# Optimization experiments

Hardware: AMD Instinct MI355X
Metric: run time of the kernel (lower is better)

## Reference

```python
import jax, jax.numpy as jnp
import numpy as np

B, S, H, HEADS, STEP = 128, 256, 128, 8, 1


def setup_inputs() -> dict:
    key = jax.random.key(0)
    ks = jax.random.split(key, 20)
    rn = lambda k, shape: jax.random.normal(k, shape, dtype=jnp.float32) * 0.1
    return {
        "A": jax.random.uniform(ks[0], (B, S, 2 * S), dtype=jnp.float32),
        "hidden": jax.random.normal(ks[1], (B, S, H), dtype=jnp.float32),
        "mask": jnp.ones((B, S), dtype=jnp.int32),
        "w_ih": rn(ks[2], (3 * H, 2 * H)),
        "w_hh": rn(ks[3], (3 * H, H)),
        "b_ih": rn(ks[4], (3 * H,)),
        "b_hh": rn(ks[5], (3 * H,)),
        "b_iah": rn(ks[6], (H,)),
        "b_oah": rn(ks[7], (H,)),
        "W_ein": rn(ks[8], (H, H)), "b_ein": rn(ks[9], (H,)),
        "W_eout": rn(ks[10], (H, H)), "b_eout": rn(ks[11], (H,)),
        "W_q0": rn(ks[12], (H, H)), "b_q0": rn(ks[13], (H,)),
        "W_q1": rn(ks[14], (H, H)), "b_q1": rn(ks[15], (H,)),
        "W_q2": rn(ks[16], (H, H)), "b_q2": rn(ks[17], (H,)),
    }


def _forward(A, hidden, mask, w_ih, w_hh, b_ih, b_hh, b_iah, b_oah,
             W_ein, b_ein, W_eout, b_eout, W_q0, b_q0, W_q1, b_q1, W_q2, b_q2):
    b, s, h = hidden.shape
    dk = h // HEADS
    # ---- GNN: gated graph propagation (GRU cell over adjacency messages) ----
    for _ in range(STEP):
        msg_in = A[:, :, :s] @ (hidden @ W_ein.T + b_ein) + b_iah    # [B,S,H]
        msg_out = A[:, :, s:] @ (hidden @ W_eout.T + b_eout) + b_oah  # [B,S,H]
        inputs = jnp.concatenate([msg_in, msg_out], axis=2)           # [B,S,2H]
        gi = inputs @ w_ih.T + b_ih                                   # [B,S,3H]
        gh = hidden @ w_hh.T + b_hh                                   # [B,S,3H]
        i_r, i_i, i_n = jnp.split(gi, 3, axis=2)
        h_r, h_i, h_n = jnp.split(gh, 3, axis=2)
        resetgate = jax.nn.sigmoid(i_r + h_r)
        inputgate = jax.nn.sigmoid(i_i + h_i)
        newgate = jnp.tanh(i_n + resetgate * h_n)
        hidden = hidden - inputgate * (hidden - newgate)
    # ---- query: hidden state of the last valid item in each session ----
    last_idx = jnp.sum(mask, axis=1) - 1
    ht1 = hidden[jnp.arange(b), last_idx]                             # [B,H]
    # ---- LastAttenion: sigmoid score + double softmax readout ----
    q0 = (ht1 @ W_q0.T + b_q0).reshape(b, HEADS, dk)                  # [B,h,dk]
    q1 = (hidden @ W_q1.T + b_q1).reshape(b, s, HEADS, dk).transpose(0, 2, 1, 3)
    q2 = (hidden @ W_q2.T + b_q2).reshape(b, s, HEADS, dk).transpose(0, 2, 1, 3)
    # q0 is expanded over the query axis, so every score row is identical
    alpha = jax.nn.sigmoid(jnp.einsum('bhd,bhjd->bhj', q0, q1))        # [B,h,S]
    alpha = jnp.broadcast_to(alpha[:, :, None, :], (b, HEADS, s, s))   # [B,h,S,S]
    alpha = jax.nn.softmax(alpha, axis=-1)
    row_keep = (mask > 0)[:, None, :, None]                            # [B,1,S,1]
    alpha = jnp.where(row_keep, alpha, -jnp.inf)
    alpha = jax.nn.softmax(2.0 * alpha, axis=1)                        # over heads
    alpha = jnp.where(row_keep, alpha, 0.0)  # guard fully-masked rows (torch would NaN)
    x = jnp.einsum('bhij,bhjd->bhid', alpha, q2)                       # [B,h,S,dk]
    x = x.transpose(0, 2, 1, 3).reshape(b, s, h)                       # [B,S,H]
    a = jnp.sum(x * mask[:, :, None].astype(x.dtype), axis=1)          # [B,H]
    return a


def reference(A, hidden, mask, w_ih, w_hh, b_ih, b_hh, b_iah, b_oah,
              W_ein, b_ein, W_eout, b_eout, W_q0, b_q0, W_q1, b_q1, W_q2, b_q2):
    return _forward(A, hidden, mask, w_ih, w_hh, b_ih, b_hh, b_iah, b_oah,
                    W_ein, b_ein, W_eout, b_eout, W_q0, b_q0, W_q1, b_q1, W_q2, b_q2)
```

## Files before the change

kernel.cpp:

```cpp
#include <hip/hip_runtime.h>
#include <cstdint>
#include <cstddef>

#define BB   128
#define SS   256
#define HH   128
#define NH   8
#define DKK  16

typedef unsigned short u16;
typedef __attribute__((ext_vector_type(8))) short   sh8;
typedef __attribute__((ext_vector_type(4))) float   f32x4;

__device__ __forceinline__ float sigmoidf_(float x) { return 1.f / (1.f + expf(-x)); }

__device__ __forceinline__ u16 f2bf(float x) {
    union { float f; unsigned int u; } v; v.f = x;
    unsigned int r = (v.u + 0x7fffu + ((v.u >> 16) & 1u)) >> 16;
    return (u16)r;
}
__device__ __forceinline__ float bf2f(u16 u) {
    union { unsigned int u; float f; } v; v.u = ((unsigned int)u) << 16;
    return v.f;
}
__device__ __forceinline__ float bflo(unsigned u) {
    union { unsigned u; float f; } v; v.u = u << 16; return v.f;
}
__device__ __forceinline__ float bfhi(unsigned u) {
    union { unsigned u; float f; } v; v.u = u & 0xffff0000u; return v.f;
}

#define BKk 32
#define PK  40
#define LP  136

template<int XMODE, int OMODE>
__global__ __launch_bounds__(256) void gemm_mfma(
    const void* __restrict__ Xa, const void* __restrict__ Xc, int ldx, int ldx1, int ksplit,
    long long sXb, long long sXh,
    const u16* __restrict__ Bw, int ldb, long long sBb, long long sBh,
    const float* __restrict__ bias,
    void* __restrict__ Out, long long ldo, long long sOb, long long sOh,
    int K, const u16* __restrict__ hid)
{
    __shared__ __align__(16) char smem[2 * 128 * PK * 2];
    u16* As = (u16*)smem;
    u16* Bs = (u16*)(smem + 128 * PK * 2);

    const int t  = threadIdx.x;
    const int bm = blockIdx.x * 128;
    const int bn = blockIdx.y * 128;
    const long long zb = blockIdx.z >> 1, zh = blockIdx.z & 1;

    const u16* Bp = Bw + zb * sBb + zh * sBh;

    const int wave = t >> 6, lane = t & 63;
    const int wr = (wave >> 1) * 64, wc = (wave & 1) * 64;
    const int fm = lane & 15, fq = lane >> 4;

    f32x4 acc[4][4] = {};

    const int r0  = t >> 2, kk0 = (t & 3) * 8;
    const int r1  = t >> 3, kk1 = (t & 7) * 4;

    uint4  px0, px1, pb0, pb1;
    float4 pf0, pf1, pf2, pf3;

#define LOADX(K0)                                                                    \
    if (XMODE == 1) {                                                                \
        const float* Xf_ = (const float*)Xa + zb * sXb + zh * sXh;                   \
        const float* xp_ = Xf_ + (long long)(bm + r1) * ldx + (K0) + kk1;            \
        pf0 = *(const float4*)(xp_);                                                 \
        pf1 = *(const float4*)(xp_ + 32LL * ldx);                                    \
        pf2 = *(const float4*)(xp_ + 64LL * ldx);                                    \
        pf3 = *(const float4*)(xp_ + 96LL * ldx);                                    \
    } else if (XMODE == 2 && (K0) >= ksplit) {                                       \
        const u16* xp_ = (const u16*)Xc + (long long)(bm + r0) * ldx1                \
                         + ((K0) - ksplit) + kk0;                                    \
        px0 = *(const uint4*)(xp_);                                                  \
        px1 = *(const uint4*)(xp_ + 64LL * ldx1);                                    \
    } else {                                                                         \
        const u16* xp_ = (const u16*)Xa + (long long)(bm + r0) * ldx + (K0) + kk0;   \
        px0 = *(const uint4*)(xp_);                                                  \
        px1 = *(const uint4*)(xp_ + 64LL * ldx);                                     \
    }

#define LOADB(K0)                                                                    \
    {                                                                                \
        const u16* bp_ = Bp + (long long)(bn + r0) * ldb + (K0) + kk0;               \
        pb0 = *(const uint4*)(bp_);                                                  \
        pb1 = *(const uint4*)(bp_ + 64LL * ldb);                                     \
    }

    LOADX(0)
    LOADB(0)

    for (int k0 = 0; k0 < K; k0 += BKk) {
        if (XMODE == 1) {
            ushort4 w0 = { f2bf(pf0.x), f2bf(pf0.y), f2bf(pf0.z), f2bf(pf0.w) };
            ushort4 w1 = { f2bf(pf1.x), f2bf(pf1.y), f2bf(pf1.z), f2bf(pf1.w) };
            ushort4 w2 = { f2bf(pf2.x), f2bf(pf2.y), f2bf(pf2.z), f2bf(pf2.w) };
            ushort4 w3 = { f2bf(pf3.x), f2bf(pf3.y), f2bf(pf3.z), f2bf(pf3.w) };
            *(ushort4*)&As[(r1     ) * PK + kk1] = w0;
            *(ushort4*)&As[(r1 + 32) * PK + kk1] = w1;
            *(ushort4*)&As[(r1 + 64) * PK + kk1] = w2;
            *(ushort4*)&As[(r1 + 96) * PK + kk1] = w3;
        } else {
            *(uint4*)&As[(r0     ) * PK + kk0] = px0;
            *(uint4*)&As[(r0 + 64) * PK + kk0] = px1;
        }
        *(uint4*)&Bs[(r0     ) * PK + kk0] = pb0;
        *(uint4*)&Bs[(r0 + 64) * PK + kk0] = pb1;
        __syncthreads();

        if (k0 + BKk < K) {
            LOADX(k0 + BKk)
            LOADB(k0 + BKk)
        }

        sh8 af[4], bfr[4];
        #pragma unroll
        for (int i = 0; i < 4; i++) af[i]  = *(const sh8*)&As[(wr + i * 16 + fm) * PK + fq * 8];
        #pragma unroll
        for (int j = 0; j < 4; j++) bfr[j] = *(const sh8*)&Bs[(wc + j * 16 + fm) * PK + fq * 8];
        #pragma unroll
        for (int i = 0; i < 4; i++)
            #pragma unroll
            for (int j = 0; j < 4; j++)
                acc[i][j] = __builtin_amdgcn_mfma_f32_16x16x32_bf16(af[i], bfr[j], acc[i][j], 0, 0, 0);
        __syncthreads();
    }
#undef LOADX
#undef LOADB

    if (OMODE != 3) {
        u16* O  = (u16*)Out + zb * sOb + zh * sOh;
        u16* Ls = (u16*)smem;
        #pragma unroll
        for (int hf = 0; hf < 2; hf++) {
            if (hf) __syncthreads();
            if (OMODE == 1) {
                if (wr == hf * 64) {
                    #pragma unroll
                    for (int i = 0; i < 4; i++)
                        #pragma unroll
                        for (int j = 0; j < 4; j++) {
                            const int cl = wc + j * 16 + fm;
                            const float bj = bias ? bias[bn + cl] : 0.f;
                            #pragma unroll
                            for (int r = 0; r < 4; r++)
                                Ls[(i * 16 + fq * 4 + r) * LP + cl] = f2bf(acc[i][j][r] + bj);
                        }
                }
            } else {
                if (wc == hf * 64) {
                    #pragma unroll
                    for (int i = 0; i < 4; i++)
                        #pragma unroll
                        for (int j = 0; j < 4; j++) {
                            const int cl = j * 16 + fm;
                            const float bj = bias ? bias[bn + hf * 64 + cl] : 0.f;
                            ushort4 w = { f2bf(acc[i][j][0] + bj), f2bf(acc[i][j][1] + bj),
                                          f2bf(acc[i][j][2] + bj), f2bf(acc[i][j][3] + bj) };
                            *(ushort4*)&Ls[cl * LP + wr + i * 16 + fq * 4] = w;
                        }
                }
            }
            __syncthreads();
            const int ro = t >> 2;
            #pragma unroll
            for (int rr = 0; rr < 4; rr++) {
                const int c0 = ((t & 3) + rr * 4) * 8;
                uint4 w = *(const uint4*)&Ls[ro * LP + c0];
                if (OMODE == 1)
                    *(uint4*)&O[(long long)(bm + hf * 64 + ro) * ldo + bn + c0] = w;
                else
                    *(uint4*)&O[(long long)(bn + hf * 64 + ro) * ldo + bm + c0] = w;
            }
        }
    } else {
        float* g4s = (float*)smem;
        const int chbase = bn >> 2;
        const int s_t = t >> 3;
        const int cq  = t & 7;
        u16* O = (u16*)Out;
        const int sbase = (wr ? 16 : 0) + fq * 4;
        #pragma unroll
        for (int i = 0; i < 4; i++) {
            #pragma unroll
            for (int j = 0; j < 4; j++) {
                const int q = wc + j * 16 + fm;
                const float bj = bias[bn + q];
                #pragma unroll
                for (int r = 0; r < 4; r++)
                    g4s[(sbase + r) * 132 + q] = acc[i][j][r] + bj;
            }
            __syncthreads();
            {
                const int grow = bm + i * 16 + (s_t < 16 ? s_t : s_t + 48);
                const ushort4 hv = *(const ushort4*)&hid[(long long)grow * HH + chbase + 4 * cq];
                const float hvv[4] = { bf2f(hv.x), bf2f(hv.y), bf2f(hv.z), bf2f(hv.w) };
                ushort4 w;
                u16* wp = (u16*)&w;
                #pragma unroll
                for (int m = 0; m < 4; m++) {
                    f32x4 gv = *(const f32x4*)&g4s[s_t * 132 + 16 * cq + 4 * m];
                    float rg = sigmoidf_(gv[0]);
                    float ig = sigmoidf_(gv[1]);
                    float ng = tanhf(gv[2] + rg * gv[3]);
                    wp[m] = f2bf(hvv[m] - ig * (hvv[m] - ng));
                }
                *(ushort4*)&O[(long long)grow * ldo + chbase + 4 * cq] = w;
            }
            __syncthreads();
        }
    }
}

__global__ __launch_bounds__(256) void k_prepw(
    const float* __restrict__ hidden, u16* __restrict__ h_bf,
    const float* __restrict__ w_ih, const float* __restrict__ w_hh,
    const float* __restrict__ b_ih, const float* __restrict__ b_hh,
    const float* __restrict__ b_iah, const float* __restrict__ b_oah,
    const float* __restrict__ W_ein, const float* __restrict__ b_ein,
    const float* __restrict__ W_eout, const float* __restrict__ b_eout,
    const float* __restrict__ W_q1, const float* __restrict__ b_q1,
    const float* __restrict__ W_q2, const float* __restrict__ b_q2,
    u16* __restrict__ W2bf, float* __restrict__ bias2,
    u16* __restrict__ Wcat, float* __restrict__ biascat,
    u16* __restrict__ Wq12, float* __restrict__ biasq12)
{
    int idx = blockIdx.x * 256 + threadIdx.x;
    {
        float4 v = ((const float4*)hidden)[idx];
        ushort4 w = { f2bf(v.x), f2bf(v.y), f2bf(v.z), f2bf(v.w) };
        ((ushort4*)h_bf)[idx] = w;
    }
    if (idx < 512 * 384) {
        int np = idx / 384, kk = idx % 384;
        int c = np >> 2, g = np & 3;
        float v;
        if (g < 2)       v = (kk < 256) ? w_ih[(g * 128 + c) * 256 + kk]
                                        : w_hh[(g * 128 + c) * 128 + kk - 256];
        else if (g == 2) v = (kk < 256) ? w_ih[(256 + c) * 256 + kk] : 0.f;
        else             v = (kk < 256) ? 0.f : w_hh[(256 + c) * 128 + kk - 256];
        W2bf[idx] = f2bf(v);
    }
    if (idx < 256 * 128) {
        int n = idx >> 7, k = idx & 127;
        Wcat[idx] = f2bf(n < 128 ? W_ein[n * 128 + k] : W_eout[(n - 128) * 128 + k]);
        Wq12[idx] = f2bf(n < 128 ? W_q1[n * 128 + k]  : W_q2[(n - 128) * 128 + k]);
    }
    if (idx < 512) {
        int np = idx, c = np >> 2, g = np & 3;
        float s;
        if (g < 2)       s = b_ih[g * 128 + c] + b_hh[g * 128 + c];
        else if (g == 2) s = b_ih[256 + c];
        else             s = b_hh[256 + c];
        if (g < 3) {
            int n = (g < 2) ? g * 128 + c : 256 + c;
            for (int k = 0; k < 128; k++)
                s += w_ih[n * 256 + k] * b_iah[k] + w_ih[n * 256 + 128 + k] * b_oah[k];
        }
        bias2[np] = s;
    }
    if (idx < 256) {
        biascat[idx] = idx < 128 ? b_ein[idx] : b_eout[idx - 128];
        biasq12[idx] = idx < 128 ? b_q1[idx]  : b_q2[idx - 128];
    }
}

__global__ __launch_bounds__(1024) void k_tail(
    const u16* __restrict__ hnew_bf, const int* __restrict__ mask,
    const u16* __restrict__ q12, const float* __restrict__ Wq0,
    const float* __restrict__ bq0, float* __restrict__ out)
{
    const int b = blockIdx.x, chb = blockIdx.y, t = threadIdx.x;
    __shared__ float red[1024];
    __shared__ float red2[1024][2];
    __shared__ float hs[HH];
    __shared__ float q0s[HH];
    __shared__ float p_s[NH][SS];
    __shared__ float w_s[NH][SS];
    __shared__ int s_nv;

    if (t < 256) {
        int v = mask[b * SS + t];
        #pragma unroll
        for (int m = 1; m < 64; m <<= 1) v += __shfl_xor(v, m, 64);
        if ((t & 63) == 0) red[t >> 6] = (float)v;
    }
    __syncthreads();
    if (t == 0) s_nv = (int)(red[0] + red[1] + red[2] + red[3]);
    __syncthreads();
    const int nv = s_nv;
    const int last = (nv - 1) & (SS - 1);

    if (t < HH) hs[t] = bf2f(hnew_bf[((size_t)b * SS + last) * HH + t]);
    __syncthreads();

    {
        const int n = t & 127, kh = t >> 7;
        const float* w = Wq0 + (size_t)n * HH + kh * 16;
        const float* h = hs + kh * 16;
        float s = 0.f;
        #pragma unroll
        for (int k = 0; k < 16; k++) s += h[k] * w[k];
        red[t] = s;
    }
    __syncthreads();
    if (t < HH) {
        float s = bq0[t];
        #pragma unroll
        for (int kh = 0; kh < 8; kh++) s += red[kh * 128 + t];
        q0s[t] = s;
    }
    __syncthreads();

    {
        const int j = t >> 2, q = t & 3;
        const u16* q1r = q12 + ((size_t)b * SS + j) * 256 + q * 32;
        uint4 va = *(const uint4*)(q1r);
        uint4 vb = *(const uint4*)(q1r + 8);
        uint4 vc = *(const uint4*)(q1r + 16);
        uint4 vd = *(const uint4*)(q1r + 24);
        const float* qa = q0s + q * 32;
        float s0 = qa[0]  * bflo(va.x) + qa[1]  * bfhi(va.x)
                 + qa[2]  * bflo(va.y) + qa[3]  * bfhi(va.y)
                 + qa[4]  * bflo(va.z) + qa[5]  * bfhi(va.z)
                 + qa[6]  * bflo(va.w) + qa[7]  * bfhi(va.w)
                 + qa[8]  * bflo(vb.x) + qa[9]  * bfhi(vb.x)
                 + qa[10] * bflo(vb.y) + qa[11] * bfhi(vb.y)
                 + qa[12] * bflo(vb.z) + qa[13] * bfhi(vb.z)
                 + qa[14] * bflo(vb.w) + qa[15] * bfhi(vb.w);
        float s1 = qa[16] * bflo(vc.x) + qa[17] * bfhi(vc.x)
                 + qa[18] * bflo(vc.y) + qa[19] * bfhi(vc.y)
                 + qa[20] * bflo(vc.z) + qa[21] * bfhi(vc.z)
                 + qa[22] * bflo(vc.w) + qa[23] * bfhi(vc.w)
                 + qa[24] * bflo(vd.x) + qa[25] * bfhi(vd.x)
                 + qa[26] * bflo(vd.y) + qa[27] * bfhi(vd.y)
                 + qa[28] * bflo(vd.z) + qa[29] * bfhi(vd.z)
                 + qa[30] * bflo(vd.w) + qa[31] * bfhi(vd.w);
        p_s[2 * q][j]     = sigmoidf_(s0);
        p_s[2 * q + 1][j] = sigmoidf_(s1);
    }
    __syncthreads();

    if (t < 256) {
        const int h = t >> 5, l = t & 31;
        float v[8], m = -1e30f;
        #pragma unroll
        for (int u = 0; u < 8; u++) { v[u] = p_s[h][l * 8 + u]; m = fmaxf(m, v[u]); }
        #pragma unroll
        for (int msk = 1; msk < 32; msk <<= 1) m = fmaxf(m, __shfl_xor(m, msk, 32));
        float sum = 0.f;
        #pragma unroll
        for (int u = 0; u < 8; u++) { v[u] = expf(v[u] - m); sum += v[u]; }
        #pragma unroll
        for (int msk = 1; msk < 32; msk <<= 1) sum += __shfl_xor(sum, msk, 32);
        const float inv = 1.f / sum;
        #pragma unroll
        for (int u = 0; u < 8; u++) p_s[h][l * 8 + u] = v[u] * inv;
    }
    __syncthreads();

    if (t < 256) {
        float e[NH], den = 0.f;
        #pragma unroll
        for (int h = 0; h < NH; h++) { e[h] = expf(2.f * p_s[h][t]); den += e[h]; }
        const float inv = 1.f / den;
        #pragma unroll
        for (int h = 0; h < NH; h++) w_s[h][t] = e[h] * inv;
    }
    __syncthreads();

    {
        const int cp = t & 31, jq = t >> 5;
        const int col = chb * 64 + cp * 2;
        const int h0 = col >> 4;
        const u16* q2b = q12 + (size_t)b * SS * 256 + 128 + col;
        float a0 = 0.f, a1 = 0.f;
        #pragma unroll
        for (int u = 0; u < 8; u++) {
            const int j = jq * 8 + u;
            const unsigned v = *(const unsigned*)&q2b[(size_t)j * 256];
            const float w = w_s[h0][j];
            a0 += w * bflo(v);
            a1 += w * bfhi(v);
        }
        red2[t][0] = a0;
        red2[t][1] = a1;
    }
    __syncthreads();
    if (t < 64) {
        const int cp2 = t >> 1, par = t & 1;
        float s = 0.f;
        #pragma unroll
        for (int q = 0; q < 32; q++) s += red2[q * 32 + cp2][par];
        out[(size_t)b * HH + chb * 64 + cp2 * 2 + par] = s * (float)nv;
    }
}

extern "C" void kernel_launch(void* const* d_in, const int* in_sizes, int n_in,
                              void* d_out, int out_size, void* d_ws, size_t ws_size,
                              hipStream_t stream)
{
    const float* A      = (const float*)d_in[0];
    const float* hidden = (const float*)d_in[1];
    const int*   mask   = (const int*)d_in[2];
    const float* w_ih   = (const float*)d_in[3];
    const float* w_hh   = (const float*)d_in[4];
    const float* b_ih   = (const float*)d_in[5];
    const float* b_hh   = (const float*)d_in[6];
    const float* b_iah  = (const float*)d_in[7];
    const float* b_oah  = (const float*)d_in[8];
    const float* W_ein  = (const float*)d_in[9];
    const float* b_ein  = (const float*)d_in[10];
    const float* W_eout = (const float*)d_in[11];
    const float* b_eout = (const float*)d_in[12];
    const float* W_q0   = (const float*)d_in[13];
    const float* b_q0   = (const float*)d_in[14];
    const float* W_q1   = (const float*)d_in[15];
    const float* b_q1   = (const float*)d_in[16];
    const float* W_q2   = (const float*)d_in[17];
    const float* b_q2   = (const float*)d_in[18];
    float* out = (float*)d_out;
    char* ws = (char*)d_ws;

    u16*   Et      = (u16*)(ws + 0);
    u16*   Mbuf    = (u16*)(ws + 16777216);
    u16*   q12bf   = (u16*)(ws + 0);
    u16*   hnew_bf = (u16*)(ws + 33554432);
    u16*   h_bf    = (u16*)(ws + 41943040);
    u16*   W2bf    = (u16*)(ws + 50331648);
    u16*   Wcat    = (u16*)(ws + 50724864);
    u16*   Wq12    = (u16*)(ws + 50790400);
    float* bias2   = (float*)(ws + 50855936);
    float* biascat = (float*)(ws + 50857984);
    float* biasq12 = (float*)(ws + 50859008);

    k_prepw<<<4096, 256, 0, stream>>>(hidden, h_bf,
                                      w_ih, w_hh, b_ih, b_hh, b_iah, b_oah,
                                      W_ein, b_ein, W_eout, b_eout,
                                      W_q1, b_q1, W_q2, b_q2,
                                      W2bf, bias2, Wcat, biascat, Wq12, biasq12);

    gemm_mfma<0, 2><<<dim3(256, 2, 1), 256, 0, stream>>>(
        h_bf, nullptr, HH, 0, 0, 0, 0,
        Wcat, HH, 0, 0, biascat,
        Et, 32768, 0, 0, HH, nullptr);

    gemm_mfma<1, 1><<<dim3(2, 1, 256), 256, 0, stream>>>(
        A, nullptr, 512, 0, 0, 131072LL, 256LL,
        Et, 32768, 256LL, 128LL * 32768LL, nullptr,
        Mbuf, 256, 65536LL, 128LL, SS, nullptr);

    gemm_mfma<2, 3><<<dim3(256, 4, 1), 256, 0, stream>>>(
        Mbuf, h_bf, 256, HH, 256, 0, 0,
        W2bf, 384, 0, 0, bias2,
        hnew_bf, HH, 0, 0, 384, h_bf);

    gemm_mfma<0, 1><<<dim3(256, 2, 1), 256, 0, stream>>>(
        hnew_bf, nullptr, HH, 0, 0, 0, 0,
        Wq12, HH, 0, 0, biasq12,
        q12bf, 256, 0, 0, HH, nullptr);

    k_tail<<<dim3(BB, 2), 1024, 0, stream>>>(hnew_bf, mask, q12bf, W_q0, b_q0, out);
}
```

Measured before the change: 221.5 us.

## Double-buffer LDS tiles and widen GEMM K-tile to 64

Doubles the K step of the MFMA GEMM main loop from 32 to 64 and keeps two LDS buffers. The next tile is committed into the idle buffer after the MFMAs, which removes one of the two barriers per iteration and halves the iteration count. The cost is much more LDS per block (about 72 KB versus 20 KB) and more registers for prefetch, which may lower occupancy. It also assumes K is a multiple of 64 and that ksplit is aligned to 64.

```diff
diff --git a/kernel.cpp b/kernel.cpp
--- a/kernel.cpp
+++ b/kernel.cpp
@@ -30,9 +30,11 @@
     union { unsigned u; float f; } v; v.u = u & 0xffff0000u; return v.f;
 }
 
-#define BKk 32
-#define PK  40
-#define LP  136
+#define BKk  64
+#define PKB  72
+#define ABUF (128 * PKB)
+#define BUFH (2 * ABUF)
+#define LP   136
 
 template<int XMODE, int OMODE>
 __global__ __launch_bounds__(256) void gemm_mfma(
@@ -43,9 +45,8 @@
     void* __restrict__ Out, long long ldo, long long sOb, long long sOh,
     int K, const u16* __restrict__ hid)
 {
-    __shared__ __align__(16) char smem[2 * 128 * PK * 2];
-    u16* As = (u16*)smem;
-    u16* Bs = (u16*)(smem + 128 * PK * 2);
+    __shared__ __align__(16) char smem[2 * BUFH * 2];
+    u16* base = (u16*)smem;
 
     const int t  = threadIdx.x;
     const int bm = blockIdx.x * 128;
@@ -60,78 +61,124 @@
 
     f32x4 acc[4][4] = {};
 
-    const int r0  = t >> 2, kk0 = (t & 3) * 8;
-    const int r1  = t >> 3, kk1 = (t & 7) * 4;
-
-    uint4  px0, px1, pb0, pb1;
-    float4 pf0, pf1, pf2, pf3;
+    const int rs = t >> 3, kcs = (t & 7) * 8;
+    const int rf = t >> 4, cf  = (t & 15) * 4;
+
+    uint4  px0, px1, px2, px3, pb0, pb1, pb2, pb3;
+    float4 pf0, pf1, pf2, pf3, pf4, pf5, pf6, pf7;
 
 #define LOADX(K0)                                                                    \
     if (XMODE == 1) {                                                                \
         const float* Xf_ = (const float*)Xa + zb * sXb + zh * sXh;                   \
-        const float* xp_ = Xf_ + (long long)(bm + r1) * ldx + (K0) + kk1;            \
+        const float* xp_ = Xf_ + (long long)(bm + rf) * ldx + (K0) + cf;             \
         pf0 = *(const float4*)(xp_);                                                 \
-        pf1 = *(const float4*)(xp_ + 32LL * ldx);                                    \
-        pf2 = *(const float4*)(xp_ + 64LL * ldx);                                    \
-        pf3 = *(const float4*)(xp_ + 96LL * ldx);                                    \
+        pf1 = *(const float4*)(xp_ +  16LL * ldx);                                   \
+        pf2 = *(const float4*)(xp_ +  32LL * ldx);                                   \
+        pf3 = *(const float4*)(xp_ +  48LL * ldx);                                   \
+        pf4 = *(const float4*)(xp_ +  64LL * ldx);                                   \
+        pf5 = *(const float4*)(xp_ +  80LL * ldx);                                   \
+        pf6 = *(const float4*)(xp_ +  96LL * ldx);                                   \
+        pf7 = *(const float4*)(xp_ + 112LL * ldx);                                   \
     } else if (XMODE == 2 && (K0) >= ksplit) {                                       \
-        const u16* xp_ = (const u16*)Xc + (long long)(bm + r0) * ldx1                \
-                         + ((K0) - ksplit) + kk0;                                    \
+        const u16* xp_ = (const u16*)Xc + (long long)(bm + rs) * ldx1               \
+                         + ((K0) - ksplit) + kcs;                                    \
         px0 = *(const uint4*)(xp_);                                                  \
-        px1 = *(const uint4*)(xp_ + 64LL * ldx1);                                    \
+        px1 = *(const uint4*)(xp_ + 32LL * ldx1);                                    \
+        px2 = *(const uint4*)(xp_ + 64LL * ldx1);                                    \
+        px3 = *(const uint4*)(xp_ + 96LL * ldx1);                                    \
     } else {                                                                         \
-        const u16* xp_ = (const u16*)Xa + (long long)(bm + r0) * ldx + (K0) + kk0;   \
+        const u16* xp_ = (const u16*)Xa + (long long)(bm + rs) * ldx + (K0) + kcs;   \
         px0 = *(const uint4*)(xp_);                                                  \
-        px1 = *(const uint4*)(xp_ + 64LL * ldx);                                     \
+        px1 = *(const uint4*)(xp_ + 32LL * ldx);                                     \
+        px2 = *(const uint4*)(xp_ + 64LL * ldx);                                     \
+        px3 = *(const uint4*)(xp_ + 96LL * ldx);                                     \
     }
 
 #define LOADB(K0)                                                                    \
     {                                                                                \
-        const u16* bp_ = Bp + (long long)(bn + r0) * ldb + (K0) + kk0;               \
+        const u16* bp_ = Bp + (long long)(bn + rs) * ldb + (K0) + kcs;               \
         pb0 = *(const uint4*)(bp_);                                                  \
-        pb1 = *(const uint4*)(bp_ + 64LL * ldb);                                     \
-    }
+        pb1 = *(const uint4*)(bp_ + 32LL * ldb);                                     \
+        pb2 = *(const uint4*)(bp_ + 64LL * ldb);                                     \
+        pb3 = *(const uint4*)(bp_ + 96LL * ldb);                                     \
+    }
+
+#define COMMIT(Ad, Bd)                                                               \
+    if (XMODE == 1) {                                                                \
+        ushort4 w0 = { f2bf(pf0.x), f2bf(pf0.y), f2bf(pf0.z), f2bf(pf0.w) };         \
+        ushort4 w1 = { f2bf(pf1.x), f2bf(pf1.y), f2bf(pf1.z), f2bf(pf1.w) };         \
+        ushort4 w2 = { f2bf(pf2.x), f2bf(pf2.y), f2bf(pf2.z), f2bf(pf2.w) };         \
+        ushort4 w3 = { f2bf(pf3.x), f2bf(pf3.y), f2bf(pf3.z), f2bf(pf3.w) };         \
+        ushort4 w4 = { f2bf(pf4.x), f2bf(pf4.y), f2bf(pf4.z), f2bf(pf4.w) };         \
+        ushort4 w5 = { f2bf(pf5.x), f2bf(pf5.y), f2bf(pf5.z), f2bf(pf5.w) };         \
+        ushort4 w6 = { f2bf(pf6.x), f2bf(pf6.y), f2bf(pf6.z), f2bf(pf6.w) };         \
+        ushort4 w7 = { f2bf(pf7.x), f2bf(pf7.y), f2bf(pf7.z), f2bf(pf7.w) };         \
+        *(ushort4*)&(Ad)[(rf      ) * PKB + cf] = w0;                                \
+        *(ushort4*)&(Ad)[(rf +  16) * PKB + cf] = w1;                                \
+        *(ushort4*)&(Ad)[(rf +  32) * PKB + cf] = w2;                                \
+        *(ushort4*)&(Ad)[(rf +  48) * PKB + cf] = w3;                                \
+        *(ushort4*)&(Ad)[(rf +  64) * PKB + cf] = w4;                                \
+        *(ushort4*)&(Ad)[(rf +  80) * PKB + cf] = w5;                                \
+        *(ushort4*)&(Ad)[(rf +  96) * PKB + cf] = w6;                                \
+        *(ushort4*)&(Ad)[(rf + 112) * PKB + cf] = w7;                                \
+    } else {                                                                         \
+        *(uint4*)&(Ad)[(rs     ) * PKB + kcs] = px0;                                 \
+        *(uint4*)&(Ad)[(rs + 32) * PKB + kcs] = px1;                                 \
+        *(uint4*)&(Ad)[(rs + 64) * PKB + kcs] = px2;                                 \
+        *(uint4*)&(Ad)[(rs + 96) * PKB + kcs] = px3;                                 \
+    }                                                                                \
+    *(uint4*)&(Bd)[(rs     ) * PKB + kcs] = pb0;                                     \
+    *(uint4*)&(Bd)[(rs + 32) * PKB + kcs] = pb1;                                     \
+    *(uint4*)&(Bd)[(rs + 64) * PKB + kcs] = pb2;                                     \
+    *(uint4*)&(Bd)[(rs + 96) * PKB + kcs] = pb3;
+
+    const int nt = K / BKk;
+    int cur = 0;
 
     LOADX(0)
     LOADB(0)
-
-    for (int k0 = 0; k0 < K; k0 += BKk) {
-        if (XMODE == 1) {
-            ushort4 w0 = { f2bf(pf0.x), f2bf(pf0.y), f2bf(pf0.z), f2bf(pf0.w) };
-            ushort4 w1 = { f2bf(pf1.x), f2bf(pf1.y), f2bf(pf1.z), f2bf(pf1.w) };
-            ushort4 w2 = { f2bf(pf2.x), f2bf(pf2.y), f2bf(pf2.z), f2bf(pf2.w) };
-            ushort4 w3 = { f2bf(pf3.x), f2bf(pf3.y), f2bf(pf3.z), f2bf(pf3.w) };
-            *(ushort4*)&As[(r1     ) * PK + kk1] = w0;
-            *(ushort4*)&As[(r1 + 32) * PK + kk1] = w1;
-            *(ushort4*)&As[(r1 + 64) * PK + kk1] = w2;
-            *(ushort4*)&As[(r1 + 96) * PK + kk1] = w3;
-        } else {
-            *(uint4*)&As[(r0     ) * PK + kk0] = px0;
-            *(uint4*)&As[(r0 + 64) * PK + kk0] = px1;
-        }
-        *(uint4*)&Bs[(r0     ) * PK + kk0] = pb0;
-        *(uint4*)&Bs[(r0 + 64) * PK + kk0] = pb1;
-        __syncthreads();
-
-        if (k0 + BKk < K) {
-            LOADX(k0 + BKk)
-            LOADB(k0 + BKk)
-        }
-
-        sh8 af[4], bfr[4];
-        #pragma unroll
-        for (int i = 0; i < 4; i++) af[i]  = *(const sh8*)&As[(wr + i * 16 + fm) * PK + fq * 8];
-        #pragma unroll
-        for (int j = 0; j < 4; j++) bfr[j] = *(const sh8*)&Bs[(wc + j * 16 + fm) * PK + fq * 8];
-        #pragma unroll
-        for (int i = 0; i < 4; i++)
+    {
+        u16* Ad = base;
+        u16* Bd = base + ABUF;
+        COMMIT(Ad, Bd)
+    }
+    __syncthreads();
+
+    for (int tt = 0; tt < nt; ++tt) {
+        if (tt + 1 < nt) {
+            LOADX((tt + 1) * BKk)
+            LOADB((tt + 1) * BKk)
+        }
+
+        const u16* Ac = base + cur * BUFH;
+        const u16* Bc = Ac + ABUF;
+        #pragma unroll
+        for (int ks = 0; ks < 2; ks++) {
+            sh8 af[4], bfr[4];
+            #pragma unroll
+            for (int i = 0; i < 4; i++)
+                af[i]  = *(const sh8*)&Ac[(wr + i * 16 + fm) * PKB + ks * 32 + fq * 8];
             #pragma unroll
             for (int j = 0; j < 4; j++)
-                acc[i][j] = __builtin_amdgcn_mfma_f32_16x16x32_bf16(af[i], bfr[j], acc[i][j], 0, 0, 0);
+                bfr[j] = *(const sh8*)&Bc[(wc + j * 16 + fm) * PKB + ks * 32 + fq * 8];
+            #pragma unroll
+            for (int i = 0; i < 4; i++)
+                #pragma unroll
+                for (int j = 0; j < 4; j++)
+                    acc[i][j] = __builtin_amdgcn_mfma_f32_16x16x32_bf16(af[i], bfr[j], acc[i][j], 0, 0, 0);
+        }
+
+        if (tt + 1 < nt) {
+            u16* Ad = base + (cur ^ 1) * BUFH;
+            u16* Bd = Ad + ABUF;
+            COMMIT(Ad, Bd)
+        }
         __syncthreads();
+        cur ^= 1;
     }
 #undef LOADX
 #undef LOADB
+#undef COMMIT
 
     if (OMODE != 3) {
         u16* O  = (u16*)Out + zb * sOb + zh * sOh;
```

After: 218.9 us. About the same (-1.1%).

## Double-buffer the GRU gate GEMM with BK=64 and drop LDS-staged epilogue

Applied to the files above, without the earlier changes.

Adds a new gemm_dbuf kernel for the fused gate GEMM (OMODE 3). It uses two shared-memory buffers with a K tile of 64, so each step needs one barrier instead of two and the next tile's global loads overlap the current MFMAs. The generic gemm_mfma epilogue for OMODE 1/2 now writes bf16 results straight from registers to global memory instead of staging them through LDS. That removes the barriers but gives less coalesced, scattered 2-byte stores. The larger LDS footprint may reduce occupancy.

```diff
diff --git a/kernel.cpp b/kernel.cpp
--- a/kernel.cpp
+++ b/kernel.cpp
@@ -32,7 +32,6 @@
 
 #define BKk 32
 #define PK  40
-#define LP  136
 
 template<int XMODE, int OMODE>
 __global__ __launch_bounds__(256) void gemm_mfma(
@@ -66,7 +65,7 @@
     uint4  px0, px1, pb0, pb1;
     float4 pf0, pf1, pf2, pf3;
 
-#define LOADX(K0)                                                                    \
+#define LOADX32(K0)                                                                  \
     if (XMODE == 1) {                                                                \
         const float* Xf_ = (const float*)Xa + zb * sXb + zh * sXh;                   \
         const float* xp_ = Xf_ + (long long)(bm + r1) * ldx + (K0) + kk1;            \
@@ -85,15 +84,15 @@
         px1 = *(const uint4*)(xp_ + 64LL * ldx);                                     \
     }
 
-#define LOADB(K0)                                                                    \
+#define LOADB32(K0)                                                                  \
     {                                                                                \
         const u16* bp_ = Bp + (long long)(bn + r0) * ldb + (K0) + kk0;               \
         pb0 = *(const uint4*)(bp_);                                                  \
         pb1 = *(const uint4*)(bp_ + 64LL * ldb);                                     \
     }
 
-    LOADX(0)
-    LOADB(0)
+    LOADX32(0)
+    LOADB32(0)
 
     for (int k0 = 0; k0 < K; k0 += BKk) {
         if (XMODE == 1) {
@@ -114,8 +113,8 @@
         __syncthreads();
 
         if (k0 + BKk < K) {
-            LOADX(k0 + BKk)
-            LOADB(k0 + BKk)
+            LOADX32(k0 + BKk)
+            LOADB32(k0 + BKk)
         }
 
         sh8 af[4], bfr[4];
@@ -130,55 +129,149 @@
                 acc[i][j] = __builtin_amdgcn_mfma_f32_16x16x32_bf16(af[i], bfr[j], acc[i][j], 0, 0, 0);
         __syncthreads();
     }
-#undef LOADX
-#undef LOADB
-
-    if (OMODE != 3) {
-        u16* O  = (u16*)Out + zb * sOb + zh * sOh;
-        u16* Ls = (u16*)smem;
-        #pragma unroll
-        for (int hf = 0; hf < 2; hf++) {
-            if (hf) __syncthreads();
+#undef LOADX32
+#undef LOADB32
+
+    #pragma unroll
+    for (int j = 0; j < 4; j++) {
+        const int col = bn + wc + j * 16 + fm;
+        const float bj = bias ? bias[col] : 0.f;
+        #pragma unroll
+        for (int i = 0; i < 4; i++) {
+            const int row0 = bm + wr + i * 16 + fq * 4;
             if (OMODE == 1) {
-                if (wr == hf * 64) {
-                    #pragma unroll
-                    for (int i = 0; i < 4; i++)
-                        #pragma unroll
-                        for (int j = 0; j < 4; j++) {
-                            const int cl = wc + j * 16 + fm;
-                            const float bj = bias ? bias[bn + cl] : 0.f;
-                            #pragma unroll
-                            for (int r = 0; r < 4; r++)
-                                Ls[(i * 16 + fq * 4 + r) * LP + cl] = f2bf(acc[i][j][r] + bj);
-                        }
-                }
+                u16* O = (u16*)Out + zb * sOb + zh * sOh;
+                #pragma unroll
+                for (int r = 0; r < 4; r++)
+                    O[(long long)(row0 + r) * ldo + col] = f2bf(acc[i][j][r] + bj);
             } else {
-                if (wc == hf * 64) {
-                    #pragma unroll
-                    for (int i = 0; i < 4; i++)
-                        #pragma unroll
-                        for (int j = 0; j < 4; j++) {
-                            const int cl = j * 16 + fm;
-                            const float bj = bias ? bias[bn + hf * 64 + cl] : 0.f;
-                            ushort4 w = { f2bf(acc[i][j][0] + bj), f2bf(acc[i][j][1] + bj),
-                                          f2bf(acc[i][j][2] + bj), f2bf(acc[i][j][3] + bj) };
-                            *(ushort4*)&Ls[cl * LP + wr + i * 16 + fq * 4] = w;
-                        }
-                }
+                u16* O = (u16*)Out + zb * sOb + zh * sOh;
+                ushort4 w = { f2bf(acc[i][j][0] + bj), f2bf(acc[i][j][1] + bj),
+                              f2bf(acc[i][j][2] + bj), f2bf(acc[i][j][3] + bj) };
+                *(ushort4*)&O[(long long)col * ldo + row0] = w;
             }
-            __syncthreads();
-            const int ro = t >> 2;
+        }
+    }
+}
+
+#define BKD  64
+#define PKB  72
+#define ABUF (128 * PKB)
+#define BUFH (2 * ABUF)
+
+template<int XMODE, int OMODE>
+__global__ __launch_bounds__(256) void gemm_dbuf(
+    const void* __restrict__ Xa, const void* __restrict__ Xc, int ldx, int ldx1, int ksplit,
+    long long sXb, long long sXh,
+    const u16* __restrict__ Bw, int ldb, long long sBb, long long sBh,
+    const float* __restrict__ bias,
+    void* __restrict__ Out, long long ldo, long long sOb, long long sOh,
+    int K, const u16* __restrict__ hid)
+{
+    __shared__ __align__(16) char smem[2 * BUFH * 2];
+    u16* base = (u16*)smem;
+
+    const int t  = threadIdx.x;
+    const int bm = blockIdx.x * 128;
+    const int bn = blockIdx.y * 128;
+    const long long zb = blockIdx.z >> 1, zh = blockIdx.z & 1;
+
+    const u16* Bp = Bw + zb * sBb + zh * sBh;
+
+    const int wave = t >> 6, lane = t & 63;
+    const int wr = (wave >> 1) * 64, wc = (wave & 1) * 64;
+    const int fm = lane & 15, fq = lane >> 4;
+
+    f32x4 acc[4][4] = {};
+
+    const int rs = t >> 3, kcs = (t & 7) * 8;
+
+    uint4  px0, px1, px2, px3, pb0, pb1, pb2, pb3;
+
+#define LOADX64(K0)                                                                  \
+    if (XMODE == 2 && (K0) >= ksplit) {                                              \
+        const u16* xp_ = (const u16*)Xc + (long long)(bm + rs) * ldx1               \
+                         + ((K0) - ksplit) + kcs;                                    \
+        px0 = *(const uint4*)(xp_);                                                  \
+        px1 = *(const uint4*)(xp_ + 32LL * ldx1);                                    \
+        px2 = *(const uint4*)(xp_ + 64LL * ldx1);                                    \
+        px3 = *(const uint4*)(xp_ + 96LL * ldx1);                                    \
+    } else {                                                                         \
+        const u16* xp_ = (const u16*)Xa + (long long)(bm + rs) * ldx + (K0) + kcs;   \
+        px0 = *(const uint4*)(xp_);                                                  \
+        px1 = *(const uint4*)(xp_ + 32LL * ldx);                                     \
+        px2 = *(const uint4*)(xp_ + 64LL * ldx);                                     \
+        px3 = *(const uint4*)(xp_ + 96LL * ldx);                                     \
+    }
+
+#define LOADB64(K0)                                                                  \
+    {                                                                                \
+        const u16* bp_ = Bp + (long long)(bn + rs) * ldb + (K0) + kcs;               \
+        pb0 = *(const uint4*)(bp_);                                                  \
+        pb1 = *(const uint4*)(bp_ + 32LL * ldb);                                     \
+        pb2 = *(const uint4*)(bp_ + 64LL * ldb);                                     \
+        pb3 = *(const uint4*)(bp_ + 96LL * ldb);                                     \
+    }
+
+#define COMMIT64(Ad, Bd)                                                             \
+    *(uint4*)&(Ad)[(rs     ) * PKB + kcs] = px0;                                     \
+    *(uint4*)&(Ad)[(rs + 32) * PKB + kcs] = px1;                                     \
+    *(uint4*)&(Ad)[(rs + 64) * PKB + kcs] = px2;                                     \
+    *(uint4*)&(Ad)[(rs + 96) * PKB + kcs] = px3;                                     \
+    *(uint4*)&(Bd)[(rs     ) * PKB + kcs] = pb0;                                     \
+    *(uint4*)&(Bd)[(rs + 32) * PKB + kcs] = pb1;                                     \
+    *(uint4*)&(Bd)[(rs + 64) * PKB + kcs] = pb2;                                     \
+    *(uint4*)&(Bd)[(rs + 96) * PKB + kcs] = pb3;
+
+    const int nt = K / BKD;
+    int cur = 0;
+
+    LOADX64(0)
+    LOADB64(0)
+    {
+        u16* Ad = base;
+        u16* Bd = base + ABUF;
+        COMMIT64(Ad, Bd)
+    }
+    __syncthreads();
+
+    for (int tt = 0; tt < nt; ++tt) {
+        if (tt + 1 < nt) {
+            LOADX64((tt + 1) * BKD)
+            LOADB64((tt + 1) * BKD)
+        }
+
+        const u16* Ac = base + cur * BUFH;
+        const u16* Bc = Ac + ABUF;
+        #pragma unroll
+        for (int ks = 0; ks < 2; ks++) {
+            sh8 af[4], bfr[4];
             #pragma unroll
-            for (int rr = 0; rr < 4; rr++) {
-                const int c0 = ((t & 3) + rr * 4) * 8;
-                uint4 w = *(const uint4*)&Ls[ro * LP + c0];
-                if (OMODE == 1)
-                    *(uint4*)&O[(long long)(bm + hf * 64 + ro) * ldo + bn + c0] = w;
-                else
-                    *(uint4*)&O[(long long)(bn + hf * 64 + ro) * ldo + bm + c0] = w;
-            }
-        }
-    } else {
+            for (int i = 0; i < 4; i++)
+                af[i]  = *(const sh8*)&Ac[(wr + i * 16 + fm) * PKB + ks * 32 + fq * 8];
+            #pragma unroll
+            for (int j = 0; j < 4; j++)
+                bfr[j] = *(const sh8*)&Bc[(wc + j * 16 + fm) * PKB + ks * 32 + fq * 8];
+            #pragma unroll
+            for (int i = 0; i < 4; i++)
+                #pragma unroll
+                for (int j = 0; j < 4; j++)
+                    acc[i][j] = __builtin_amdgcn_mfma_f32_16x16x32_bf16(af[i], bfr[j], acc[i][j], 0, 0, 0);
+        }
+
+        if (tt + 1 < nt) {
+            u16* Ad = base + (cur ^ 1) * BUFH;
+            u16* Bd = Ad + ABUF;
+            COMMIT64(Ad, Bd)
+        }
+        __syncthreads();
+        cur ^= 1;
+    }
+#undef LOADX64
+#undef LOADB64
+#undef COMMIT64
+
+    {
         float* g4s = (float*)smem;
         const int chbase = bn >> 2;
         const int s_t = t >> 3;
@@ -455,7 +548,7 @@
         Et, 32768, 256LL, 128LL * 32768LL, nullptr,
         Mbuf, 256, 65536LL, 128LL, SS, nullptr);
 
-    gemm_mfma<2, 3><<<dim3(256, 4, 1), 256, 0, stream>>>(
+    gemm_dbuf<2, 3><<<dim3(256, 4, 1), 256, 0, stream>>>(
         Mbuf, h_bf, 256, HH, 256, 0, 0,
         W2bf, 384, 0, 0, bias2,
         hnew_bf, HH, 0, 0, 384, h_bf);
```

Result: faster. 215.3 us (-2.8%).

## Fuse adjacency message GEMM with GRU gate GEMM into one kernel

Applied to the files above, without the earlier changes.

Replaces the separate A@E message GEMM and the gate GEMM with a single kernel that keeps each 64-row message tile in LDS and immediately multiplies it by the GRU weights, applying the gate nonlinearity in the epilogue. This removes the Mbuf round trip through global memory and one launch. The generic GEMM epilogue also drops its LDS-staged coalesced store in favour of direct per-element global stores. In exchange the fused kernel uses about 80KB of LDS per block, which limits occupancy, and the direct stores are less coalesced.

```diff
diff --git a/kernel.cpp b/kernel.cpp
--- a/kernel.cpp
+++ b/kernel.cpp
@@ -32,7 +32,6 @@
 
 #define BKk 32
 #define PK  40
-#define LP  136
 
 template<int XMODE, int OMODE>
 __global__ __launch_bounds__(256) void gemm_mfma(
@@ -66,7 +65,7 @@
     uint4  px0, px1, pb0, pb1;
     float4 pf0, pf1, pf2, pf3;
 
-#define LOADX(K0)                                                                    \
+#define LOADX32(K0)                                                                  \
     if (XMODE == 1) {                                                                \
         const float* Xf_ = (const float*)Xa + zb * sXb + zh * sXh;                   \
         const float* xp_ = Xf_ + (long long)(bm + r1) * ldx + (K0) + kk1;            \
@@ -85,15 +84,15 @@
         px1 = *(const uint4*)(xp_ + 64LL * ldx);                                     \
     }
 
-#define LOADB(K0)                                                                    \
+#define LOADB32(K0)                                                                  \
     {                                                                                \
         const u16* bp_ = Bp + (long long)(bn + r0) * ldb + (K0) + kk0;               \
         pb0 = *(const uint4*)(bp_);                                                  \
         pb1 = *(const uint4*)(bp_ + 64LL * ldb);                                     \
     }
 
-    LOADX(0)
-    LOADB(0)
+    LOADX32(0)
+    LOADB32(0)
 
     for (int k0 = 0; k0 < K; k0 += BKk) {
         if (XMODE == 1) {
@@ -114,8 +113,8 @@
         __syncthreads();
 
         if (k0 + BKk < K) {
-            LOADX(k0 + BKk)
-            LOADB(k0 + BKk)
+            LOADX32(k0 + BKk)
+            LOADB32(k0 + BKk)
         }
 
         sh8 af[4], bfr[4];
@@ -130,91 +129,228 @@
                 acc[i][j] = __builtin_amdgcn_mfma_f32_16x16x32_bf16(af[i], bfr[j], acc[i][j], 0, 0, 0);
         __syncthreads();
     }
-#undef LOADX
-#undef LOADB
-
-    if (OMODE != 3) {
-        u16* O  = (u16*)Out + zb * sOb + zh * sOh;
-        u16* Ls = (u16*)smem;
-        #pragma unroll
-        for (int hf = 0; hf < 2; hf++) {
-            if (hf) __syncthreads();
+#undef LOADX32
+#undef LOADB32
+
+    #pragma unroll
+    for (int j = 0; j < 4; j++) {
+        const int col = bn + wc + j * 16 + fm;
+        const float bj = bias ? bias[col] : 0.f;
+        #pragma unroll
+        for (int i = 0; i < 4; i++) {
+            const int row0 = bm + wr + i * 16 + fq * 4;
             if (OMODE == 1) {
-                if (wr == hf * 64) {
-                    #pragma unroll
-                    for (int i = 0; i < 4; i++)
-                        #pragma unroll
-                        for (int j = 0; j < 4; j++) {
-                            const int cl = wc + j * 16 + fm;
-                            const float bj = bias ? bias[bn + cl] : 0.f;
-                            #pragma unroll
-                            for (int r = 0; r < 4; r++)
-                                Ls[(i * 16 + fq * 4 + r) * LP + cl] = f2bf(acc[i][j][r] + bj);
-                        }
-                }
-            } else {
-                if (wc == hf * 64) {
-                    #pragma unroll
-                    for (int i = 0; i < 4; i++)
-                        #pragma unroll
-                        for (int j = 0; j < 4; j++) {
-                            const int cl = j * 16 + fm;
-                            const float bj = bias ? bias[bn + hf * 64 + cl] : 0.f;
-                            ushort4 w = { f2bf(acc[i][j][0] + bj), f2bf(acc[i][j][1] + bj),
-                                          f2bf(acc[i][j][2] + bj), f2bf(acc[i][j][3] + bj) };
-                            *(ushort4*)&Ls[cl * LP + wr + i * 16 + fq * 4] = w;
-                        }
-                }
-            }
-            __syncthreads();
-            const int ro = t >> 2;
-            #pragma unroll
-            for (int rr = 0; rr < 4; rr++) {
-                const int c0 = ((t & 3) + rr * 4) * 8;
-                uint4 w = *(const uint4*)&Ls[ro * LP + c0];
-                if (OMODE == 1)
-                    *(uint4*)&O[(long long)(bm + hf * 64 + ro) * ldo + bn + c0] = w;
-                else
-                    *(uint4*)&O[(long long)(bn + hf * 64 + ro) * ldo + bm + c0] = w;
-            }
-        }
-    } else {
-        float* g4s = (float*)smem;
-        const int chbase = bn >> 2;
-        const int s_t = t >> 3;
-        const int cq  = t & 7;
-        u16* O = (u16*)Out;
-        const int sbase = (wr ? 16 : 0) + fq * 4;
-        #pragma unroll
-        for (int i = 0; i < 4; i++) {
-            #pragma unroll
-            for (int j = 0; j < 4; j++) {
-                const int q = wc + j * 16 + fm;
-                const float bj = bias[bn + q];
+                u16* O = (u16*)Out + zb * sOb + zh * sOh;
                 #pragma unroll
                 for (int r = 0; r < 4; r++)
-                    g4s[(sbase + r) * 132 + q] = acc[i][j][r] + bj;
+                    O[(long long)(row0 + r) * ldo + col] = f2bf(acc[i][j][r] + bj);
+            } else {
+                u16* O = (u16*)Out + zb * sOb + zh * sOh;
+                ushort4 w = { f2bf(acc[i][j][0] + bj), f2bf(acc[i][j][1] + bj),
+                              f2bf(acc[i][j][2] + bj), f2bf(acc[i][j][3] + bj) };
+                *(ushort4*)&O[(long long)col * ldo + row0] = w;
+            }
+        }
+    }
+}
+
+#define MGP 392
+#define SGP 40
+
+__global__ __launch_bounds__(256) void k_msg_gates(
+    const float* __restrict__ A,
+    const u16*   __restrict__ Et,
+    const u16*   __restrict__ h_bf,
+    const u16*   __restrict__ W2bf,
+    const float* __restrict__ bias2,
+    u16*         __restrict__ hnew)
+{
+    __shared__ __align__(16) char smem[80896];
+    u16*   Mloc = (u16*)smem;
+    u16*   As   = (u16*)(smem + 50176);
+    u16*   Bs   = (u16*)(smem + 60416);
+    u16*   Ws   = (u16*)(smem + 50176);
+    float* Gs   = (float*)(smem + 50176);
+
+    const int t  = threadIdx.x;
+    const int r0 = blockIdx.x * 64;
+    const int b  = blockIdx.x >> 2;
+
+    const int wave = t >> 6, lane = t & 63;
+    const int fm = lane & 15, fq = lane >> 4;
+    const int zh = wave >> 1;
+    const int wn = wave * 64;
+
+    const f32x4 fz = { 0.f, 0.f, 0.f, 0.f };
+    f32x4 acc[4][4];
+
+    {
+        const int hrow = t >> 2, cb = (t & 3) * 32;
+        const u16* hp = h_bf + (long long)(r0 + hrow) * HH + cb;
+        uint4 h0 = *(const uint4*)(hp);
+        uint4 h1 = *(const uint4*)(hp + 8);
+        uint4 h2 = *(const uint4*)(hp + 16);
+        uint4 h3 = *(const uint4*)(hp + 24);
+        *(uint4*)&Mloc[hrow * MGP + 256 + cb     ] = h0;
+        *(uint4*)&Mloc[hrow * MGP + 256 + cb + 8 ] = h1;
+        *(uint4*)&Mloc[hrow * MGP + 256 + cb + 16] = h2;
+        *(uint4*)&Mloc[hrow * MGP + 256 + cb + 24] = h3;
+    }
+
+    const int arow = t >> 1, acol = (t & 1) * 16;
+    const int arl  = arow & 63, ah = arow >> 6;
+
+    float4 qa0, qa1, qa2, qa3;
+    uint4  qe0, qe1, qe2, qe3;
+
+#define LOADP1(K0)                                                                   \
+    {                                                                                \
+        const float* ap_ = A + (long long)(r0 + arl) * 512 + ah * 256 + (K0) + acol; \
+        qa0 = *(const float4*)(ap_);                                                 \
+        qa1 = *(const float4*)(ap_ + 4);                                             \
+        qa2 = *(const float4*)(ap_ + 8);                                             \
+        qa3 = *(const float4*)(ap_ + 12);                                            \
+        const u16* ep_ = Et + (long long)t * 32768 + b * 256 + (K0);                 \
+        qe0 = *(const uint4*)(ep_);                                                  \
+        qe1 = *(const uint4*)(ep_ + 8);                                              \
+        qe2 = *(const uint4*)(ep_ + 16);                                             \
+        qe3 = *(const uint4*)(ep_ + 24);                                             \
+    }
+
+#define COMMITP1                                                                     \
+    {                                                                                \
+        ushort4 a0 = { f2bf(qa0.x), f2bf(qa0.y), f2bf(qa0.z), f2bf(qa0.w) };         \
+        ushort4 a1 = { f2bf(qa1.x), f2bf(qa1.y), f2bf(qa1.z), f2bf(qa1.w) };         \
+        ushort4 a2 = { f2bf(qa2.x), f2bf(qa2.y), f2bf(qa2.z), f2bf(qa2.w) };         \
+        ushort4 a3 = { f2bf(qa3.x), f2bf(qa3.y), f2bf(qa3.z), f2bf(qa3.w) };         \
+        *(ushort4*)&As[arow * SGP + acol     ] = a0;                                 \
+        *(ushort4*)&As[arow * SGP + acol + 4 ] = a1;                                 \
+        *(ushort4*)&As[arow * SGP + acol + 8 ] = a2;                                 \
+        *(ushort4*)&As[arow * SGP + acol + 12] = a3;                                 \
+        *(uint4*)&Bs[t * SGP     ] = qe0;                                            \
+        *(uint4*)&Bs[t * SGP + 8 ] = qe1;                                            \
+        *(uint4*)&Bs[t * SGP + 16] = qe2;                                            \
+        *(uint4*)&Bs[t * SGP + 24] = qe3;                                            \
+    }
+
+    #pragma unroll
+    for (int i = 0; i < 4; i++)
+        #pragma unroll
+        for (int j = 0; j < 4; j++) acc[i][j] = fz;
+
+    LOADP1(0)
+    for (int k0 = 0; k0 < 256; k0 += 32) {
+        COMMITP1
+        __syncthreads();
+        if (k0 + 32 < 256) LOADP1(k0 + 32)
+        sh8 af[4], bfr[4];
+        #pragma unroll
+        for (int i = 0; i < 4; i++)
+            af[i]  = *(const sh8*)&As[(zh * 64 + i * 16 + fm) * SGP + fq * 8];
+        #pragma unroll
+        for (int j = 0; j < 4; j++)
+            bfr[j] = *(const sh8*)&Bs[(wn + j * 16 + fm) * SGP + fq * 8];
+        #pragma unroll
+        for (int i = 0; i < 4; i++)
+            #pragma unroll
+            for (int j = 0; j < 4; j++)
+                acc[i][j] = __builtin_amdgcn_mfma_f32_16x16x32_bf16(af[i], bfr[j], acc[i][j], 0, 0, 0);
+        __syncthreads();
+    }
+#undef LOADP1
+#undef COMMITP1
+
+    #pragma unroll
+    for (int i = 0; i < 4; i++)
+        #pragma unroll
+        for (int j = 0; j < 4; j++)
+            #pragma unroll
+            for (int r = 0; r < 4; r++)
+                Mloc[(i * 16 + fq * 4 + r) * MGP + wn + j * 16 + fm] = f2bf(acc[i][j][r]);
+    __syncthreads();
+
+    uint4 qw0, qw1, qw2, qw3;
+
+#define LOADP2(GB, K0)                                                               \
+    {                                                                                \
+        const u16* wp_ = W2bf + (long long)((GB) + t) * 384 + (K0);                  \
+        qw0 = *(const uint4*)(wp_);                                                  \
+        qw1 = *(const uint4*)(wp_ + 8);                                              \
+        qw2 = *(const uint4*)(wp_ + 16);                                             \
+        qw3 = *(const uint4*)(wp_ + 24);                                             \
+    }
+
+#define COMMITP2                                                                     \
+    {                                                                                \
+        *(uint4*)&Ws[t * SGP     ] = qw0;                                            \
+        *(uint4*)&Ws[t * SGP + 8 ] = qw1;                                            \
+        *(uint4*)&Ws[t * SGP + 16] = qw2;                                            \
+        *(uint4*)&Ws[t * SGP + 24] = qw3;                                            \
+    }
+
+    for (int p = 0; p < 2; p++) {
+        const int gb = p * 256;
+        #pragma unroll
+        for (int i = 0; i < 4; i++)
+            #pragma unroll
+            for (int j = 0; j < 4; j++) acc[i][j] = fz;
+
+        LOADP2(gb, 0)
+        for (int k0 = 0; k0 < 384; k0 += 32) {
+            COMMITP2
+            __syncthreads();
+            if (k0 + 32 < 384) LOADP2(gb, k0 + 32)
+            sh8 af[4], bfr[4];
+            #pragma unroll
+            for (int i = 0; i < 4; i++)
+                af[i]  = *(const sh8*)&Mloc[(i * 16 + fm) * MGP + k0 + fq * 8];
+            #pragma unroll
+            for (int j = 0; j < 4; j++)
+                bfr[j] = *(const sh8*)&Ws[(wn + j * 16 + fm) * SGP + fq * 8];
+            #pragma unroll
+            for (int i = 0; i < 4; i++)
+                #pragma unroll
+                for (int j = 0; j < 4; j++)
+                    acc[i][j] = __builtin_amdgcn_mfma_f32_16x16x32_bf16(af[i], bfr[j], acc[i][j], 0, 0, 0);
+            __syncthreads();
+        }
+
+        const float bj0 = bias2[gb + wn + 0 * 16 + fm];
+        const float bj1 = bias2[gb + wn + 1 * 16 + fm];
+        const float bj2 = bias2[gb + wn + 2 * 16 + fm];
+        const float bj3 = bias2[gb + wn + 3 * 16 + fm];
+        #pragma unroll
+        for (int i = 0; i < 4; i++) {
+            #pragma unroll
+            for (int r = 0; r < 4; r++) {
+                Gs[(fq * 4 + r) * 260 + wn + 0 * 16 + fm] = acc[i][0][r] + bj0;
+                Gs[(fq * 4 + r) * 260 + wn + 1 * 16 + fm] = acc[i][1][r] + bj1;
+                Gs[(fq * 4 + r) * 260 + wn + 2 * 16 + fm] = acc[i][2][r] + bj2;
+                Gs[(fq * 4 + r) * 260 + wn + 3 * 16 + fm] = acc[i][3][r] + bj3;
             }
             __syncthreads();
             {
-                const int grow = bm + i * 16 + (s_t < 16 ? s_t : s_t + 48);
-                const ushort4 hv = *(const ushort4*)&hid[(long long)grow * HH + chbase + 4 * cq];
+                const int row_l = t >> 4, c0 = (t & 15) * 4;
+                const long long grow = r0 + i * 16 + row_l;
+                const ushort4 hv = *(const ushort4*)&h_bf[grow * HH + p * 64 + c0];
                 const float hvv[4] = { bf2f(hv.x), bf2f(hv.y), bf2f(hv.z), bf2f(hv.w) };
                 ushort4 w;
                 u16* wp = (u16*)&w;
                 #pragma unroll
                 for (int m = 0; m < 4; m++) {
-                    f32x4 gv = *(const f32x4*)&g4s[s_t * 132 + 16 * cq + 4 * m];
+                    f32x4 gv = *(const f32x4*)&Gs[row_l * 260 + (t & 15) * 16 + 4 * m];
                     float rg = sigmoidf_(gv[0]);
                     float ig = sigmoidf_(gv[1]);
                     float ng = tanhf(gv[2] + rg * gv[3]);
                     wp[m] = f2bf(hvv[m] - ig * (hvv[m] - ng));
                 }
-                *(ushort4*)&O[(long long)grow * ldo + chbase + 4 * cq] = w;
+                *(ushort4*)&hnew[grow * HH + p * 64 + c0] = w;
             }
             __syncthreads();
         }
     }
+#undef LOADP2
+#undef COMMITP2
 }
 
 __global__ __launch_bounds__(256) void k_prepw(
@@ -428,7 +564,6 @@
     char* ws = (char*)d_ws;
 
     u16*   Et      = (u16*)(ws + 0);
-    u16*   Mbuf    = (u16*)(ws + 16777216);
     u16*   q12bf   = (u16*)(ws + 0);
     u16*   hnew_bf = (u16*)(ws + 33554432);
     u16*   h_bf    = (u16*)(ws + 41943040);
@@ -450,15 +585,7 @@
         Wcat, HH, 0, 0, biascat,
         Et, 32768, 0, 0, HH, nullptr);
 
-    gemm_mfma<1, 1><<<dim3(2, 1, 256), 256, 0, stream>>>(
-        A, nullptr, 512, 0, 0, 131072LL, 256LL,
-        Et, 32768, 256LL, 128LL * 32768LL, nullptr,
-        Mbuf, 256, 65536LL, 128LL, SS, nullptr);
-
-    gemm_mfma<2, 3><<<dim3(256, 4, 1), 256, 0, stream>>>(
-        Mbuf, h_bf, 256, HH, 256, 0, 0,
-        W2bf, 384, 0, 0, bias2,
-        hnew_bf, HH, 0, 0, 384, h_bf);
+    k_msg_gates<<<512, 256, 0, stream>>>(A, Et, h_bf, W2bf, bias2, hnew_bf);
 
     gemm_mfma<0, 1><<<dim3(256, 2, 1), 256, 0, stream>>>(
         hnew_bf, nullptr, HH, 0, 0, 0, 0,
```

Result: no change. 224.0 us (+1.1%).
